# Kernel tuning notes

Hardware: AMD Instinct MI355X
Metric: run time of the kernel (lower is better)

The kernel has to match this reference:

```python
import jax, jax.numpy as jnp
import numpy as np

HEAD_DIM = 64
MASK_PENALTY = 1000000.0


def setup_inputs() -> dict:
    key = jax.random.key(0)
    kq, kk, kv, ki = jax.random.split(key, 4)
    B, H, S, D = 32, 16, 512, HEAD_DIM
    E, CAP = 8, 4  # n_experts = hidden(1024)//128, capacity per expert
    Q = jax.random.normal(kq, (B, H, S, D), dtype=jnp.float32)
    K = jax.random.normal(kk, (B, H, S, D), dtype=jnp.float32)
    V = jax.random.normal(kv, (B, H, S, D), dtype=jnp.float32)
    idx_list = jax.random.randint(ki, (E, CAP), 0, B)  # per-expert routed batch indices
    mask = jnp.ones((B, S), dtype=jnp.float32)
    return {"Q": Q, "K": K, "V": V, "idx_list": idx_list, "mask": mask}


def reference(Q, K, V, idx_list, mask):
    # Per-expert grouped attention: gather routed batch rows, QK^T, masked
    # softmax, AV. Dropout is identity in eval mode.
    scale = 1.0 / jnp.sqrt(jnp.asarray(HEAD_DIM, dtype=Q.dtype))

    def expert_attn(idx_e):
        q = Q[idx_e]            # [cap, H, S, D]
        k = K[idx_e]
        v = V[idx_e]
        m = mask[idx_e]         # [cap, S]
        dot = jnp.einsum('bhsd,bhtd->bhst', q, k) * scale
        dot = dot - MASK_PENALTY * (1.0 - m[:, None, None, :])
        p = jax.nn.softmax(dot, axis=-1)
        return jnp.einsum('bhst,bhtd->bhsd', p, v)  # [cap, H, S, D]

    X = jax.vmap(expert_attn)(idx_list)  # [E, cap, H, S, D]
    return X
```

## Files before the change

### kernel.cpp

```cpp
#include <hip/hip_runtime.h>
#include <math.h>


typedef _Float16 f16x8 __attribute__((ext_vector_type(8)));
typedef _Float16 f16x4 __attribute__((ext_vector_type(4)));
typedef _Float16 f16x2 __attribute__((ext_vector_type(2)));
typedef float    f32x4 __attribute__((ext_vector_type(4)));

#define MFMA16(a, b, c) __builtin_amdgcn_mfma_f32_16x16x32_f16((a), (b), (c), 0, 0, 0)

constexpr int Hh = 16;
constexpr int Ss = 512;
constexpr int Dd = 64;
constexpr int QB = 256;
constexpr int KVR = 128;
constexpr int NR = Ss / KVR;
constexpr float QS = 0.125f * 1.44269504088896f;
constexpr float BM = 1000000.0f * 1.44269504088896f;

union U8 { f16x8 v; f16x2 h[4]; };

__device__ __forceinline__ int SW64(int row, int col) {
  return row * 64 + (col ^ ((row & 7) << 3));
}
__device__ __forceinline__ int SW128(int row, int col) {
  return row * 128 + (col ^ ((row & 7) << 3));
}

__device__ __forceinline__ f16x2 pkrtz(float a, float b) {
  auto t = __builtin_amdgcn_cvt_pkrtz(a, b);
  return *(f16x2*)&t;
}

__global__ __launch_bounds__(512) void sparse_attn_kernel(
    const float* __restrict__ Q, const float* __restrict__ K,
    const float* __restrict__ V, const int* __restrict__ idx,
    const float* __restrict__ mask, float* __restrict__ out) {
  const int tid  = threadIdx.x;
  const int lane = tid & 63;
  const int wv   = tid >> 6;
  const int r    = lane & 15;
  const int g    = lane >> 4;

  const int phys = blockIdx.x;
  const int G    = (phys & 7) | ((phys >> 4) << 3);
  const int qb   = (phys >> 3) & 1;
  const int h    = G & 15;
  const int ec   = G >> 4;
  const int b    = idx[ec];

  __shared__ _Float16 Ks[128 * 64];
  __shared__ _Float16 VTs[64 * 128];
  __shared__ float    biasS[Ss];

  const size_t bh = ((size_t)b * Hh + h) * (size_t)Ss * Dd;
  const float* Qb = Q + bh;
  const float* Kb = K + bh;
  const float* Vb = V + bh;
  const float* mrow = mask + (size_t)b * Ss;

  biasS[tid] = mrow[tid] * BM - BM;

  const int q0 = qb * QB + wv * 32;

  f16x8 qf[2][2];
#pragma unroll
  for (int mi = 0; mi < 2; ++mi)
#pragma unroll
    for (int kk = 0; kk < 2; ++kk) {
      const float* qp = Qb + (size_t)(q0 + mi * 16 + r) * Dd + kk * 32 + g * 8;
      float4 x0 = *(const float4*)qp;
      float4 x1 = *(const float4*)(qp + 4);
      U8 u;
      u.h[0] = pkrtz(x0.x * QS, x0.y * QS);
      u.h[1] = pkrtz(x0.z * QS, x0.w * QS);
      u.h[2] = pkrtz(x1.x * QS, x1.y * QS);
      u.h[3] = pkrtz(x1.z * QS, x1.w * QS);
      qf[mi][kk] = u.v;
    }

  f16x8 ones;
#pragma unroll
  for (int e = 0; e < 8; ++e) ones[e] = (_Float16)1.0f;

  f32x4 oacc[2][4];
#pragma unroll
  for (int mi = 0; mi < 2; ++mi)
#pragma unroll
    for (int nj = 0; nj < 4; ++nj) oacc[mi][nj] = (f32x4){0.f, 0.f, 0.f, 0.f};
  f32x4 lacc[2] = {(f32x4){0.f, 0.f, 0.f, 0.f}, (f32x4){0.f, 0.f, 0.f, 0.f}};

  float4 kx0[2], kx1[2];
  float  vv[2][8];

#define KV_ISSUE(KV0)                                                        \
  {                                                                          \
    _Pragma("unroll")                                                        \
    for (int it = 0; it < 2; ++it) {                                         \
      int j = it * 512 + tid;                                                \
      const float* kp_ = Kb + (size_t)((KV0) + (j >> 3)) * Dd + (j & 7) * 8; \
      kx0[it] = *(const float4*)kp_;                                         \
      kx1[it] = *(const float4*)(kp_ + 4);                                   \
    }                                                                        \
    _Pragma("unroll")                                                        \
    for (int it = 0; it < 2; ++it) {                                         \
      int oct = tid >> 6;                                                    \
      int kb1 = (oct >> 2) * 16 + (oct & 3) * 4 + it * 64;                   \
      const float* vp = Vb + (size_t)((KV0) + kb1) * Dd + (tid & 63);        \
      _Pragma("unroll")                                                      \
      for (int jj = 0; jj < 4; ++jj) {                                       \
        vv[it][jj]     = vp[(size_t)jj * Dd];                                \
        vv[it][jj + 4] = vp[(size_t)(jj + 32) * Dd];                         \
      }                                                                      \
    }                                                                        \
  }

#define STAGE_WRITE()                                                        \
  {                                                                          \
    _Pragma("unroll")                                                        \
    for (int it = 0; it < 2; ++it) {                                         \
      int j = it * 512 + tid;                                                \
      U8 u;                                                                  \
      u.h[0] = pkrtz(kx0[it].x, kx0[it].y);                                  \
      u.h[1] = pkrtz(kx0[it].z, kx0[it].w);                                  \
      u.h[2] = pkrtz(kx1[it].x, kx1[it].y);                                  \
      u.h[3] = pkrtz(kx1[it].z, kx1[it].w);                                  \
      *(f16x8*)&Ks[SW64(j >> 3, (j & 7) * 8)] = u.v;                         \
    }                                                                        \
    _Pragma("unroll")                                                        \
    for (int it = 0; it < 2; ++it) {                                         \
      int dim = tid & 63;                                                    \
      int cb  = it * 8 + (tid >> 6);                    \
      U8 u;                                                                  \
      u.h[0] = pkrtz(vv[it][0], vv[it][1]);                                  \
      u.h[1] = pkrtz(vv[it][2], vv[it][3]);                                  \
      u.h[2] = pkrtz(vv[it][4], vv[it][5]);                                  \
      u.h[3] = pkrtz(vv[it][6], vv[it][7]);                                  \
      *(f16x8*)&VTs[SW128(dim, cb * 8)] = u.v;                               \
    }                                                                        \
  }

  KV_ISSUE(0)

  for (int t = 0; t < NR; ++t) {
    const int kv0 = t * KVR;
    if (t) __syncthreads();

    STAGE_WRITE()
    if (t < NR - 1) KV_ISSUE(kv0 + KVR)
    __syncthreads();

#pragma unroll
    for (int half = 0; half < 2; ++half) {
      const int kh = kv0 + half * 64;

      f32x4 bv[4];
#pragma unroll
      for (int nj = 0; nj < 4; ++nj)
        bv[nj] = *(const f32x4*)&biasS[kh + nj * 16 + g * 4];

      f32x4 sf[2][4];
#pragma unroll
      for (int nj = 0; nj < 4; ++nj) { sf[0][nj] = bv[nj]; sf[1][nj] = bv[nj]; }
      __builtin_amdgcn_s_setprio(1);
#pragma unroll
      for (int nj = 0; nj < 4; ++nj)
#pragma unroll
        for (int kk = 0; kk < 2; ++kk) {
          f16x8 kf = *(const f16x8*)&Ks[SW64(half * 64 + nj * 16 + r,
                                             kk * 32 + g * 8)];
          sf[0][nj] = MFMA16(kf, qf[0][kk], sf[0][nj]);
          sf[1][nj] = MFMA16(kf, qf[1][kk], sf[1][nj]);
        }
      __builtin_amdgcn_s_setprio(0);

      f16x8 pf[2][2];
#pragma unroll
      for (int mi = 0; mi < 2; ++mi) {
        float p[4][4];
#pragma unroll
        for (int nj = 0; nj < 4; ++nj)
#pragma unroll
          for (int rg = 0; rg < 4; ++rg)
            p[nj][rg] = __builtin_amdgcn_exp2f(sf[mi][nj][rg]);
#pragma unroll
        for (int kk = 0; kk < 2; ++kk) {
          U8 u;
          u.h[0] = pkrtz(p[kk][0], p[kk][1]);
          u.h[1] = pkrtz(p[kk][2], p[kk][3]);
          u.h[2] = pkrtz(p[kk + 2][0], p[kk + 2][1]);
          u.h[3] = pkrtz(p[kk + 2][2], p[kk + 2][3]);
          pf[mi][kk] = u.v;
        }
      }

      __builtin_amdgcn_s_setprio(1);
#pragma unroll
      for (int kk = 0; kk < 2; ++kk) {
        lacc[0] = MFMA16(pf[0][kk], ones, lacc[0]);
        lacc[1] = MFMA16(pf[1][kk], ones, lacc[1]);
#pragma unroll
        for (int nj = 0; nj < 4; ++nj) {
          f16x8 vf = *(const f16x8*)&VTs[SW128(nj * 16 + r,
                                               half * 64 + kk * 32 + g * 8)];
          oacc[0][nj] = MFMA16(pf[0][kk], vf, oacc[0][nj]);
          oacc[1][nj] = MFMA16(pf[1][kk], vf, oacc[1][nj]);
        }
      }
      __builtin_amdgcn_s_setprio(0);
    }
  }

  float* ob = out + ((size_t)ec * Hh + h) * (size_t)Ss * Dd;
#pragma unroll
  for (int mi = 0; mi < 2; ++mi) {
    float i4[4];
#pragma unroll
    for (int rg = 0; rg < 4; ++rg) i4[rg] = 1.0f / lacc[mi][rg];
#pragma unroll
    for (int nj = 0; nj < 4; ++nj)
#pragma unroll
      for (int rg = 0; rg < 4; ++rg) {
        int row = q0 + mi * 16 + g * 4 + rg;
        int dim = nj * 16 + r;
        ob[(size_t)row * Dd + dim] = oacc[mi][nj][rg] * i4[rg];
      }
  }
}

extern "C" void kernel_launch(void* const* d_in, const int* in_sizes, int n_in,
                              void* d_out, int out_size, void* d_ws, size_t ws_size,
                              hipStream_t stream) {
  const float* Q    = (const float*)d_in[0];
  const float* K    = (const float*)d_in[1];
  const float* V    = (const float*)d_in[2];
  const int*   idx  = (const int*)d_in[3];
  const float* mask = (const float*)d_in[4];
  float* out = (float*)d_out;
  dim3 grid(1024), block(512);
  hipLaunchKernelGGL(sparse_attn_kernel, grid, block, 0, stream,
                     Q, K, V, idx, mask, out);
}
```

Measured before the change: 66.16 us.

## Software-pipeline QK and PV halves and compute row sums on VALU

Restructures each KV tile into two explicitly interleaved halves, so the second half's QK^T MFMAs are issued before the first half's PV MFMAs, letting softmax exp work overlap matrix-core work. The row-sum accumulation moves from extra MFMAs against a ones vector to VALU adds plus cross-lane shuffles at the end. The V^T shared buffer is split into two 64x64 swizzled halves. This removes four MFMAs per half-tile but adds VALU adds, shuffles and register pressure from keeping two score tiles live.

After: 132.4 us. 100% more time.

```diff
diff --git a/kernel.cpp b/kernel.cpp
--- a/kernel.cpp
+++ b/kernel.cpp
@@ -3,7 +3,6 @@
 
 
 typedef _Float16 f16x8 __attribute__((ext_vector_type(8)));
-typedef _Float16 f16x4 __attribute__((ext_vector_type(4)));
 typedef _Float16 f16x2 __attribute__((ext_vector_type(2)));
 typedef float    f32x4 __attribute__((ext_vector_type(4)));
 
@@ -22,9 +21,6 @@
 
 __device__ __forceinline__ int SW64(int row, int col) {
   return row * 64 + (col ^ ((row & 7) << 3));
-}
-__device__ __forceinline__ int SW128(int row, int col) {
-  return row * 128 + (col ^ ((row & 7) << 3));
 }
 
 __device__ __forceinline__ f16x2 pkrtz(float a, float b) {
@@ -50,7 +46,7 @@
   const int b    = idx[ec];
 
   __shared__ _Float16 Ks[128 * 64];
-  __shared__ _Float16 VTs[64 * 128];
+  __shared__ _Float16 VTs[2][64 * 64];
   __shared__ float    biasS[Ss];
 
   const size_t bh = ((size_t)b * Hh + h) * (size_t)Ss * Dd;
@@ -79,16 +75,12 @@
       qf[mi][kk] = u.v;
     }
 
-  f16x8 ones;
-#pragma unroll
-  for (int e = 0; e < 8; ++e) ones[e] = (_Float16)1.0f;
-
   f32x4 oacc[2][4];
 #pragma unroll
   for (int mi = 0; mi < 2; ++mi)
 #pragma unroll
     for (int nj = 0; nj < 4; ++nj) oacc[mi][nj] = (f32x4){0.f, 0.f, 0.f, 0.f};
-  f32x4 lacc[2] = {(f32x4){0.f, 0.f, 0.f, 0.f}, (f32x4){0.f, 0.f, 0.f, 0.f}};
+  float l_acc[2] = {0.f, 0.f};
 
   float4 kx0[2], kx1[2];
   float  vv[2][8];
@@ -129,14 +121,38 @@
     }                                                                        \
     _Pragma("unroll")                                                        \
     for (int it = 0; it < 2; ++it) {                                         \
-      int dim = tid & 63;                                                    \
-      int cb  = it * 8 + (tid >> 6);                    \
       U8 u;                                                                  \
       u.h[0] = pkrtz(vv[it][0], vv[it][1]);                                  \
       u.h[1] = pkrtz(vv[it][2], vv[it][3]);                                  \
       u.h[2] = pkrtz(vv[it][4], vv[it][5]);                                  \
       u.h[3] = pkrtz(vv[it][6], vv[it][7]);                                  \
-      *(f16x8*)&VTs[SW128(dim, cb * 8)] = u.v;                               \
+      *(f16x8*)&VTs[it][SW64(tid & 63, (tid >> 6) * 8)] = u.v;               \
+    }                                                                        \
+  }
+
+#define SOFTMAX(SF, PF)                                                      \
+  {                                                                          \
+    _Pragma("unroll")                                                        \
+    for (int mi = 0; mi < 2; ++mi) {                                         \
+      float p[4][4];                                                         \
+      _Pragma("unroll")                                                      \
+      for (int nj = 0; nj < 4; ++nj)                                         \
+        _Pragma("unroll")                                                    \
+        for (int rg = 0; rg < 4; ++rg)                                       \
+          p[nj][rg] = __builtin_amdgcn_exp2f(SF[mi][nj][rg]);                \
+      _Pragma("unroll")                                                      \
+      for (int kk = 0; kk < 2; ++kk) {                                       \
+        U8 u;                                                                \
+        u.h[0] = pkrtz(p[kk][0], p[kk][1]);                                  \
+        u.h[1] = pkrtz(p[kk][2], p[kk][3]);                                  \
+        u.h[2] = pkrtz(p[kk + 2][0], p[kk + 2][1]);                          \
+        u.h[3] = pkrtz(p[kk + 2][2], p[kk + 2][3]);                          \
+        PF[mi][kk] = u.v;                                                    \
+      }                                                                      \
+      l_acc[mi] += ((p[0][0] + p[0][1]) + (p[0][2] + p[0][3])) +             \
+                   ((p[1][0] + p[1][1]) + (p[1][2] + p[1][3])) +             \
+                   ((p[2][0] + p[2][1]) + (p[2][2] + p[2][3])) +             \
+                   ((p[3][0] + p[3][1]) + (p[3][2] + p[3][3]));              \
     }                                                                        \
   }
 
@@ -150,73 +166,77 @@
     if (t < NR - 1) KV_ISSUE(kv0 + KVR)
     __syncthreads();
 
-#pragma unroll
-    for (int half = 0; half < 2; ++half) {
-      const int kh = kv0 + half * 64;
-
-      f32x4 bv[4];
-#pragma unroll
-      for (int nj = 0; nj < 4; ++nj)
-        bv[nj] = *(const f32x4*)&biasS[kh + nj * 16 + g * 4];
-
-      f32x4 sf[2][4];
-#pragma unroll
-      for (int nj = 0; nj < 4; ++nj) { sf[0][nj] = bv[nj]; sf[1][nj] = bv[nj]; }
-      __builtin_amdgcn_s_setprio(1);
-#pragma unroll
-      for (int nj = 0; nj < 4; ++nj)
-#pragma unroll
-        for (int kk = 0; kk < 2; ++kk) {
-          f16x8 kf = *(const f16x8*)&Ks[SW64(half * 64 + nj * 16 + r,
-                                             kk * 32 + g * 8)];
-          sf[0][nj] = MFMA16(kf, qf[0][kk], sf[0][nj]);
-          sf[1][nj] = MFMA16(kf, qf[1][kk], sf[1][nj]);
-        }
-      __builtin_amdgcn_s_setprio(0);
-
-      f16x8 pf[2][2];
-#pragma unroll
-      for (int mi = 0; mi < 2; ++mi) {
-        float p[4][4];
-#pragma unroll
-        for (int nj = 0; nj < 4; ++nj)
-#pragma unroll
-          for (int rg = 0; rg < 4; ++rg)
-            p[nj][rg] = __builtin_amdgcn_exp2f(sf[mi][nj][rg]);
-#pragma unroll
-        for (int kk = 0; kk < 2; ++kk) {
-          U8 u;
-          u.h[0] = pkrtz(p[kk][0], p[kk][1]);
-          u.h[1] = pkrtz(p[kk][2], p[kk][3]);
-          u.h[2] = pkrtz(p[kk + 2][0], p[kk + 2][1]);
-          u.h[3] = pkrtz(p[kk + 2][2], p[kk + 2][3]);
-          pf[mi][kk] = u.v;
-        }
-      }
-
-      __builtin_amdgcn_s_setprio(1);
+    f32x4 sf0[2][4];
+#pragma unroll
+    for (int nj = 0; nj < 4; ++nj) {
+      f32x4 bv = *(const f32x4*)&biasS[kv0 + nj * 16 + g * 4];
+      sf0[0][nj] = bv; sf0[1][nj] = bv;
+    }
+    __builtin_amdgcn_s_setprio(1);
+#pragma unroll
+    for (int nj = 0; nj < 4; ++nj)
 #pragma unroll
       for (int kk = 0; kk < 2; ++kk) {
-        lacc[0] = MFMA16(pf[0][kk], ones, lacc[0]);
-        lacc[1] = MFMA16(pf[1][kk], ones, lacc[1]);
-#pragma unroll
-        for (int nj = 0; nj < 4; ++nj) {
-          f16x8 vf = *(const f16x8*)&VTs[SW128(nj * 16 + r,
-                                               half * 64 + kk * 32 + g * 8)];
-          oacc[0][nj] = MFMA16(pf[0][kk], vf, oacc[0][nj]);
-          oacc[1][nj] = MFMA16(pf[1][kk], vf, oacc[1][nj]);
-        }
-      }
-      __builtin_amdgcn_s_setprio(0);
+        f16x8 kf = *(const f16x8*)&Ks[SW64(nj * 16 + r, kk * 32 + g * 8)];
+        sf0[0][nj] = MFMA16(kf, qf[0][kk], sf0[0][nj]);
+        sf0[1][nj] = MFMA16(kf, qf[1][kk], sf0[1][nj]);
+      }
+    __builtin_amdgcn_s_setprio(0);
+
+    f16x8 pf0[2][2];
+    SOFTMAX(sf0, pf0)
+
+    f32x4 sf1[2][4];
+#pragma unroll
+    for (int nj = 0; nj < 4; ++nj) {
+      f32x4 bv = *(const f32x4*)&biasS[kv0 + 64 + nj * 16 + g * 4];
+      sf1[0][nj] = bv; sf1[1][nj] = bv;
     }
+    __builtin_amdgcn_s_setprio(1);
+#pragma unroll
+    for (int nj = 0; nj < 4; ++nj)
+#pragma unroll
+      for (int kk = 0; kk < 2; ++kk) {
+        f16x8 kf = *(const f16x8*)&Ks[SW64(64 + nj * 16 + r, kk * 32 + g * 8)];
+        sf1[0][nj] = MFMA16(kf, qf[0][kk], sf1[0][nj]);
+        sf1[1][nj] = MFMA16(kf, qf[1][kk], sf1[1][nj]);
+      }
+
+#pragma unroll
+    for (int kk = 0; kk < 2; ++kk)
+#pragma unroll
+      for (int nj = 0; nj < 4; ++nj) {
+        f16x8 vf = *(const f16x8*)&VTs[0][SW64(nj * 16 + r, kk * 32 + g * 8)];
+        oacc[0][nj] = MFMA16(pf0[0][kk], vf, oacc[0][nj]);
+        oacc[1][nj] = MFMA16(pf0[1][kk], vf, oacc[1][nj]);
+      }
+    __builtin_amdgcn_s_setprio(0);
+
+    f16x8 pf1[2][2];
+    SOFTMAX(sf1, pf1)
+
+    __builtin_amdgcn_s_setprio(1);
+#pragma unroll
+    for (int kk = 0; kk < 2; ++kk)
+#pragma unroll
+      for (int nj = 0; nj < 4; ++nj) {
+        f16x8 vf = *(const f16x8*)&VTs[1][SW64(nj * 16 + r, kk * 32 + g * 8)];
+        oacc[0][nj] = MFMA16(pf1[0][kk], vf, oacc[0][nj]);
+        oacc[1][nj] = MFMA16(pf1[1][kk], vf, oacc[1][nj]);
+      }
+    __builtin_amdgcn_s_setprio(0);
   }
 
   float* ob = out + ((size_t)ec * Hh + h) * (size_t)Ss * Dd;
 #pragma unroll
   for (int mi = 0; mi < 2; ++mi) {
+    float rs = l_acc[mi];
+    rs += __shfl_xor(rs, 16);
+    rs += __shfl_xor(rs, 32);
+    float linv = 1.0f / rs;
     float i4[4];
 #pragma unroll
-    for (int rg = 0; rg < 4; ++rg) i4[rg] = 1.0f / lacc[mi][rg];
+    for (int rg = 0; rg < 4; ++rg) i4[rg] = __shfl(linv, g * 4 + rg, 16);
 #pragma unroll
     for (int nj = 0; nj < 4; ++nj)
 #pragma unroll
```
